# Performance work log

Hardware: AMD Instinct MI355X
Metric: run time of the kernel (lower is better)

## Reference

```python
import jax, jax.numpy as jnp
import numpy as np

B, S, D, H, V, DFF, L, MAXLEN = 256, 64, 1024, 16, 64, 4096, 8, 64
HD = D // H
SCALE = HD ** -0.5
EPS = 1e-5


def _ln(x, g, b):
    m = jnp.mean(x, axis=-1, keepdims=True)
    v = jnp.mean((x - m) ** 2, axis=-1, keepdims=True)
    return (x - m) * jax.lax.rsqrt(v + EPS) * g + b


def setup_inputs() -> dict:
    key = jax.random.key(0)
    ks = jax.random.split(key, 12)
    n = lambda k, shape: jax.random.normal(k, shape, jnp.float32) * 0.02
    return {
        "x": jax.random.randint(ks[0], (B, S), 0, V + 1),
        "step": 0,
        "token_embed": n(ks[1], (V + 1, D)),
        "step_embed": n(ks[2], (MAXLEN, D)),
        "qkv_w": n(ks[3], (L, 3 * D, D)),
        "qkv_b": jnp.zeros((L, 3 * D), jnp.float32),
        "out_w": n(ks[4], (L, D, D)),
        "out_b": jnp.zeros((L, D), jnp.float32),
        "rel_bias": n(ks[5], (L, 2 * MAXLEN - 1)),
        "w1": n(ks[6], (L, DFF, D)),
        "b1": jnp.zeros((L, DFF), jnp.float32),
        "w2": n(ks[7], (L, D, DFF)),
        "b2": jnp.zeros((L, D), jnp.float32),
        "ln1_g": jnp.ones((L, D), jnp.float32),
        "ln1_b": jnp.zeros((L, D), jnp.float32),
        "ln2_g": jnp.ones((L, D), jnp.float32),
        "ln2_b": jnp.zeros((L, D), jnp.float32),
        "lno_g": jnp.ones((D,), jnp.float32),
        "lno_b": jnp.zeros((D,), jnp.float32),
        "pol_w": n(ks[8], (V, D)),
        "pol_b": jnp.zeros((V,), jnp.float32),
        "val_w": n(ks[9], (1, D)),
        "val_b": jnp.zeros((1,), jnp.float32),
    }


def _forward(x, step, token_embed, step_embed, qkv_w, qkv_b, out_w, out_b,
             rel_bias, w1, b1, w2, b2, ln1_g, ln1_b, ln2_g, ln2_b,
             lno_g, lno_b, pol_w, pol_b, val_w, val_b):
    h = token_embed[x]  # [B,S,D]
    step_idx = min(int(step), MAXLEN - 1)
    h = h + step_embed[step_idx][None, None, :]

    pos = jnp.arange(S)
    rel_idx = jnp.clip(pos[:, None] - pos[None, :] + (MAXLEN - 1), 0, 2 * MAXLEN - 2)  # [S,S]

    def layer(h, p):
        qw, qb, ow, ob, rb, w1_, b1_, w2_, b2_, g1, be1, g2, be2 = p
        qkv = h @ qw.T + qb  # [B,S,3D]
        qkv = qkv.reshape(B, S, 3, H, HD).transpose(2, 0, 3, 1, 4)
        q, k, v = qkv[0], qkv[1], qkv[2]  # [B,H,S,HD]
        scores = jnp.einsum('bhqd,bhkd->bhqk', q, k) * SCALE + rb[rel_idx][None, None]
        probs = jax.nn.softmax(scores, axis=-1)
        attn = jnp.einsum('bhqk,bhkd->bhqd', probs, v)  # [B,H,S,HD]
        attn = attn.transpose(0, 2, 1, 3).reshape(B, S, D) @ ow.T + ob
        h = _ln(h + attn, g1, be1)
        ffn = jax.nn.gelu(h @ w1_.T + b1_, approximate=False) @ w2_.T + b2_
        h = _ln(h + ffn, g2, be2)
        return h, None

    h, _ = jax.lax.scan(layer, h, (qkv_w, qkv_b, out_w, out_b, rel_bias,
                                   w1, b1, w2, b2, ln1_g, ln1_b, ln2_g, ln2_b))
    h = _ln(h, lno_g, lno_b)
    pooled = h.mean(axis=1)  # [B,D]
    policy = pooled @ pol_w.T + pol_b  # [B,V]
    value = pooled @ val_w.T + val_b   # [B,1]
    return policy, value, h


def reference(x, step, token_embed, step_embed, qkv_w, qkv_b, out_w, out_b,
              rel_bias, w1, b1, w2, b2, ln1_g, ln1_b, ln2_g, ln2_b,
              lno_g, lno_b, pol_w, pol_b, val_w, val_b):
    return _forward(x, step, token_embed, step_embed, qkv_w, qkv_b, out_w, out_b,
                    rel_bias, w1, b1, w2, b2, ln1_g, ln1_b, ln2_g, ln2_b,
                    lno_g, lno_b, pol_w, pol_b, val_w, val_b)
```

## Files before the change

kernel.cpp:

```cpp
#include <hip/hip_runtime.h>
#include <math.h>

typedef _Float16 f16;
typedef _Float16 f16x8 __attribute__((ext_vector_type(8)));
typedef _Float16 f16x4 __attribute__((ext_vector_type(4)));
typedef float floatx4 __attribute__((ext_vector_type(4)));

#define BATCH 256
#define SEQ 64
#define DMODEL 1024
#define NHEAD 16
#define HDIM 64
#define VOCAB 64
#define DFF 4096
#define NLAYER 8
#define MS (BATCH*SEQ)

#define GPTR(p) ((const __attribute__((address_space(1))) void*)(p))
#define LPTR(p) ((__attribute__((address_space(3))) void*)(p))
#define GLDS(s, d) __builtin_amdgcn_global_load_lds(GPTR(s), LPTR(d), 16, 0, 0)
#define BARR() asm volatile("s_barrier" ::: "memory")

__device__ __forceinline__ floatx4 mfma16(f16x8 a, f16x8 b, floatx4 c) {
    return __builtin_amdgcn_mfma_f32_16x16x32_f16(a, b, c, 0, 0, 0);
}

__device__ __forceinline__ float gelu_f(float x) {
    float x3 = x * x * x;
    float y = -1.5957691216f * fmaf(0.044715f, x3, x);
    return x / (1.f + __expf(y));
}

__global__ __launch_bounds__(256) void embed_k(const int* __restrict__ x, const int* __restrict__ step,
                                               const float* __restrict__ tok, const float* __restrict__ se,
                                               f16* __restrict__ r) {
    int row = blockIdx.x;
    int t = threadIdx.x;
    int id = x[row];
    int si = min(max(step[0], 0), 63);
    float4 a = ((const float4*)(tok + (size_t)id * DMODEL))[t];
    float4 b = ((const float4*)(se + (size_t)si * DMODEL))[t];
    f16x4 hv; hv[0] = (f16)(a.x + b.x); hv[1] = (f16)(a.y + b.y);
    hv[2] = (f16)(a.z + b.z); hv[3] = (f16)(a.w + b.w);
    ((f16x4*)(r + (size_t)row * DMODEL))[t] = hv;
}

__global__ __launch_bounds__(256) void cvt4_k(const float* __restrict__ qw, const float* __restrict__ ow,
                                              const float* __restrict__ w1, const float* __restrict__ w2,
                                              f16* __restrict__ dq, f16* __restrict__ dO,
                                              f16* __restrict__ d1, f16* __restrict__ d2) {
    int gid = blockIdx.x * 256 + threadIdx.x;
    const float4* s; f16x4* d; int off;
    if (gid < 786432)        { s = (const float4*)qw; d = (f16x4*)dq; off = gid; }
    else if (gid < 1048576)  { s = (const float4*)ow; d = (f16x4*)dO; off = gid - 786432; }
    else if (gid < 2097152)  { s = (const float4*)w1; d = (f16x4*)d1; off = gid - 1048576; }
    else                     { s = (const float4*)w2; d = (f16x4*)d2; off = gid - 2097152; }
    float4 v = s[off];
    f16x4 o; o[0] = (f16)v.x; o[1] = (f16)v.y; o[2] = (f16)v.z; o[3] = (f16)v.w;
    d[off] = o;
}

template<int MODE>
__global__ __launch_bounds__(512, 2) void gemm8_k(const f16* __restrict__ A, const f16* __restrict__ Bw,
                                                  const float* __restrict__ bias, f16* __restrict__ Cb,
                                                  int M, int N, int K) {
    __shared__ f16 smem[65536];

    const int tid = threadIdx.x;
    const int lane = tid & 63;
    const int wave = tid >> 6;
    const int wm = wave >> 2, wn = wave & 3;
    const int lr = lane & 15, lg = lane >> 4;
    const int sa = lr & 7;

    const unsigned nx = gridDim.x;
    const unsigned nwg = nx * gridDim.y;
    unsigned flat = blockIdx.y * nx + blockIdx.x;
    flat = (flat & 7u) * (nwg >> 3) + (flat >> 3);
    const int m0 = (int)(flat / nx) * 256;
    const int n0 = (int)(flat % nx) * 256;

    floatx4 acc[8][4] = {};

    const int srow = tid >> 3;
    const int scb = (tid & 7) ^ (srow & 7);
    const f16* Ag = A + (size_t)(m0 + srow) * K + scb * 8;
    const f16* Bg = Bw + (size_t)(n0 + srow) * K + scb * 8;
    const int ldsw = wave * 512;

#define STAGE_A(bi, tt) do { const f16* _p = Ag + (size_t)(tt) * 64;                       \
    f16* _d = smem + (bi) * 32768 + ldsw;                                                  \
    GLDS(_p, _d); GLDS(_p + 64 * (size_t)K, _d + 4096);                                    \
    GLDS(_p + 128 * (size_t)K, _d + 8192); GLDS(_p + 192 * (size_t)K, _d + 12288); } while (0)
#define STAGE_BH(bi, tt, h) do { const f16* _p = Bg + (size_t)(tt) * 64 + (size_t)(h) * 128 * K; \
    f16* _d = smem + (bi) * 32768 + 16384 + (h) * 8192 + ldsw;                             \
    GLDS(_p, _d); GLDS(_p + 64 * (size_t)K, _d + 4096); } while (0)

    const int NT = K >> 6;

    STAGE_A(0, 0);
    STAGE_BH(0, 0, 0); STAGE_BH(0, 0, 1);
    STAGE_BH(1, 1, 0); STAGE_BH(1, 1, 1);
    asm volatile("s_waitcnt vmcnt(4)" ::: "memory");
    BARR();

    for (int t = 0; t < NT; ++t) {
        const int pofs = (t & 1) << 15;
        const f16* Ab = smem + pofs;
        const f16* Bb = smem + pofs + 16384;
        f16x8 bf[4][2];

        {
            f16x8 af[2][2];
#pragma unroll
            for (int kh = 0; kh < 2; ++kh)
#pragma unroll
                for (int i = 0; i < 2; ++i)
                    af[i][kh] = *(const f16x8*)(Ab + (wm * 128 + i * 16 + lr) * 64 + (((kh * 4 + lg) ^ sa) << 3));
#pragma unroll
            for (int kh = 0; kh < 2; ++kh)
#pragma unroll
                for (int ni = 0; ni < 4; ++ni)
                    bf[ni][kh] = *(const f16x8*)(Bb + (wn * 64 + ni * 16 + lr) * 64 + (((kh * 4 + lg) ^ sa) << 3));
            if (t + 1 < NT) STAGE_A((t & 1) ^ 1, t + 1);
            asm volatile("s_waitcnt lgkmcnt(8)" ::: "memory");
            BARR();
            asm volatile("s_waitcnt lgkmcnt(0)" ::: "memory");
            __builtin_amdgcn_sched_barrier(0);
            __builtin_amdgcn_s_setprio(1);
#pragma unroll
            for (int kh = 0; kh < 2; ++kh)
#pragma unroll
                for (int i = 0; i < 2; ++i)
#pragma unroll
                    for (int ni = 0; ni < 4; ++ni)
                        acc[i][ni] = mfma16(af[i][kh], bf[ni][kh], acc[i][ni]);
            __builtin_amdgcn_s_setprio(0);
            BARR();
        }
#pragma unroll
        for (int q = 1; q < 4; ++q) {
            f16x8 af[2][2];
#pragma unroll
            for (int kh = 0; kh < 2; ++kh)
#pragma unroll
                for (int i = 0; i < 2; ++i)
                    af[i][kh] = *(const f16x8*)(Ab + (wm * 128 + q * 32 + i * 16 + lr) * 64 + (((kh * 4 + lg) ^ sa) << 3));
            if (q == 1 && t + 2 < NT) STAGE_BH(t & 1, t + 2, 0);
            if (q == 2 && t + 2 < NT) STAGE_BH(t & 1, t + 2, 1);
            BARR();
            asm volatile("s_waitcnt lgkmcnt(0)" ::: "memory");
            __builtin_amdgcn_sched_barrier(0);
            __builtin_amdgcn_s_setprio(1);
#pragma unroll
            for (int kh = 0; kh < 2; ++kh)
#pragma unroll
                for (int i = 0; i < 2; ++i)
#pragma unroll
                    for (int ni = 0; ni < 4; ++ni)
                        acc[q * 2 + i][ni] = mfma16(af[i][kh], bf[ni][kh], acc[q * 2 + i][ni]);
            __builtin_amdgcn_s_setprio(0);
            if (q == 3) {
                if (t + 2 < NT)      { asm volatile("s_waitcnt vmcnt(4)" ::: "memory"); }
                else if (t + 1 < NT) { asm volatile("s_waitcnt vmcnt(0)" ::: "memory"); }
            }
            BARR();
        }
    }
#undef STAGE_A
#undef STAGE_BH

    f16* scr = smem + wave * 8192;
    float bsv[4];
#pragma unroll
    for (int ni = 0; ni < 4; ++ni) bsv[ni] = bias[n0 + wn * 64 + ni * 16 + lr];
#pragma unroll
    for (int mi = 0; mi < 8; ++mi)
#pragma unroll
        for (int ni = 0; ni < 4; ++ni)
#pragma unroll
            for (int j = 0; j < 4; ++j) {
                int rr = mi * 16 + lg * 4 + j;
                int cc = ni * 16 + lr;
                float v = acc[mi][ni][j] + bsv[ni];
                if (MODE == 1) v = gelu_f(v);
                scr[rr * 64 + (((cc >> 3) ^ (rr & 7)) * 8) + (cc & 7)] = (f16)v;
            }
#pragma unroll
    for (int half = 0; half < 2; ++half) {
        int r2 = half * 64 + lane;
        int gr = m0 + wm * 128 + r2;
        f16* dst = Cb + (size_t)gr * N + n0 + wn * 64;
#pragma unroll
        for (int i = 0; i < 8; ++i) {
            f16x8 v = *(const f16x8*)(scr + r2 * 64 + ((i ^ (r2 & 7)) * 8));
            *(f16x8*)(dst + i * 8) = v;
        }
    }
}

__global__ __launch_bounds__(256, 2) void gemm2_k(const f16* __restrict__ A, const f16* __restrict__ Bw,
                                                  const float* __restrict__ bias,
                                                  const f16* __restrict__ Rres, f16* __restrict__ ResOut,
                                                  float2* __restrict__ Part,
                                                  int M, int N, int K) {
    __shared__ f16 smem[40960];

    const int tid = threadIdx.x;
    const int lane = tid & 63;
    const int wave = tid >> 6;
    const int wm = wave >> 1, wn = wave & 1;
    const int lr = lane & 15, lg = lane >> 4;
    const int sa = lr & 7;

    const unsigned nx = gridDim.x;
    const unsigned nwg = nx * gridDim.y;
    unsigned flat = blockIdx.y * nx + blockIdx.x;
    flat = (flat & 7u) * (nwg >> 3) + (flat >> 3);
    const int m0 = (int)(flat / nx) * 128;
    const int n0 = (int)(flat % nx) * 128;

    floatx4 acc[4][4] = {};

    const int srow = tid >> 3;
    const int scbs = (tid & 7) ^ (srow & 7);
    const f16* Asrc = A + (size_t)(m0 + srow) * K + scbs * 8;
    const f16* Bsrc = Bw + (size_t)(n0 + srow) * K + scbs * 8;
    const int ldsw = wave * 512;

#define STAGEA(bi, tt) do { const f16* _a = Asrc + (size_t)(tt) * 64;                      \
    f16* _l = smem + (bi) * 8192 + ldsw;                                                   \
    GLDS(_a, _l); GLDS(_a + 32 * (size_t)K, _l + 2048);                                    \
    GLDS(_a + 64 * (size_t)K, _l + 4096); GLDS(_a + 96 * (size_t)K, _l + 6144); } while (0)
#define STAGEB(bi, tt) do { const f16* _b = Bsrc + (size_t)(tt) * 64;                      \
    f16* _l = smem + 16384 + (bi) * 8192 + ldsw;                                           \
    GLDS(_b, _l); GLDS(_b + 32 * (size_t)K, _l + 2048);                                    \
    GLDS(_b + 64 * (size_t)K, _l + 4096); GLDS(_b + 96 * (size_t)K, _l + 6144); } while (0)

    const int NT = K >> 6;

    STAGEA(0, 0);
    STAGEB(0, 0);
    STAGEB(1, 1);
    asm volatile("s_waitcnt vmcnt(4)" ::: "memory");
    __builtin_amdgcn_s_barrier();

    int ab = 0, bb = 0;
    for (int t = 0; t < NT; ++t) {
        if (t + 1 < NT) STAGEA(ab ^ 1, t + 1);
        if (t + 2 < NT) { int b2 = bb + 2; if (b2 >= 3) b2 -= 3; STAGEB(b2, t + 2); }

        const f16* Ab = smem + ab * 8192;
        const f16* Bb = smem + 16384 + bb * 8192;
        f16x8 af[8], bf[8];
#pragma unroll
        for (int kh = 0; kh < 2; ++kh)
#pragma unroll
            for (int mi = 0; mi < 4; ++mi)
                af[kh * 4 + mi] = *(const f16x8*)(Ab + (wm * 64 + mi * 16 + lr) * 64
                                                  + (((kh * 4 + lg) ^ sa) << 3));
#pragma unroll
        for (int kh = 0; kh < 2; ++kh)
#pragma unroll
            for (int ni = 0; ni < 4; ++ni)
                bf[kh * 4 + ni] = *(const f16x8*)(Bb + (wn * 64 + ni * 16 + lr) * 64
                                                  + (((kh * 4 + lg) ^ sa) << 3));

        __builtin_amdgcn_s_setprio(1);
#pragma unroll
        for (int kh = 0; kh < 2; ++kh)
#pragma unroll
            for (int mi = 0; mi < 4; ++mi)
#pragma unroll
                for (int ni = 0; ni < 4; ++ni)
                    acc[mi][ni] = mfma16(af[kh * 4 + mi], bf[kh * 4 + ni], acc[mi][ni]);
        __builtin_amdgcn_s_setprio(0);

        if (t + 2 < NT)      { asm volatile("s_waitcnt vmcnt(4)" ::: "memory"); }
        else if (t + 1 < NT) { asm volatile("s_waitcnt vmcnt(0)" ::: "memory"); }
        __builtin_amdgcn_s_barrier();

        ab ^= 1;
        bb = (bb == 2) ? 0 : bb + 1;
    }
#undef STAGEA
#undef STAGEB

    float bsv[4];
#pragma unroll
    for (int ni = 0; ni < 4; ++ni) bsv[ni] = bias[n0 + wn * 64 + ni * 16 + lr];
    f16* scr = smem + wave * 4096;
#pragma unroll
    for (int mi = 0; mi < 4; ++mi)
#pragma unroll
        for (int ni = 0; ni < 4; ++ni)
#pragma unroll
            for (int j = 0; j < 4; ++j) {
                int rr = mi * 16 + lg * 4 + j;
                int cc = ni * 16 + lr;
                scr[rr * 64 + (((cc >> 3) ^ (rr & 7)) * 8) + (cc & 7)]
                    = (f16)(acc[mi][ni][j] + bsv[ni]);
            }
    int gr = m0 + wm * 64 + lane;
    const f16* rrow = Rres + (size_t)gr * N + n0 + wn * 64;
    f16* orow = ResOut + (size_t)gr * N + n0 + wn * 64;
    float s = 0.f, ss = 0.f;
#pragma unroll
    for (int i = 0; i < 8; ++i) {
        f16x8 a = *(const f16x8*)(scr + lane * 64 + ((i ^ (lane & 7)) * 8));
        f16x8 rv = *(const f16x8*)(rrow + i * 8);
        f16x8 o;
#pragma unroll
        for (int k = 0; k < 8; ++k) {
            float v = (float)a[k] + (float)rv[k];
            s += v; ss += v * v;
            o[k] = (f16)v;
        }
        *(f16x8*)(orow + i * 8) = o;
    }
    float* red = (float*)(smem + 16384);
    if (wn == 1) { red[(wm * 64 + lane) * 2] = s; red[(wm * 64 + lane) * 2 + 1] = ss; }
    __syncthreads();
    if (wn == 0) {
        float s2 = red[(wm * 64 + lane) * 2], ss2 = red[(wm * 64 + lane) * 2 + 1];
        Part[(size_t)gr * (N >> 7) + (n0 >> 7)] = float2{s + s2, ss + ss2};
    }
}

__global__ __launch_bounds__(64) void attn_k(const f16* __restrict__ qkv, const float* __restrict__ rb,
                                             f16* __restrict__ ctx) {
    const int hh = blockIdx.x;
    const int bb = blockIdx.y;
    const int lane = threadIdx.x;
    __shared__ float rbs[128];
    __shared__ f16 Vt[64][72];
    __shared__ f16 Pl[64][72];

    for (int i = lane; i < 127; i += 64) rbs[i] = rb[i];

    const f16* vrow = qkv + (size_t)(bb * 64 + lane) * 3072 + 2048 + hh * 64;
#pragma unroll
    for (int i = 0; i < 8; ++i) {
        f16x8 v = *(const f16x8*)(vrow + i * 8);
#pragma unroll
        for (int j = 0; j < 8; ++j) Vt[i * 8 + j][lane] = v[j];
    }
    __syncthreads();

    const int lr = lane & 15, lg = lane >> 4;
    floatx4 sacc[4][4] = {};
    const f16* qbase = qkv + (size_t)(bb * 64) * 3072 + hh * 64;
#pragma unroll
    for (int kk = 0; kk < 64; kk += 32) {
        f16x8 qa[4], kb[4];
#pragma unroll
        for (int mf = 0; mf < 4; ++mf)
            qa[mf] = *(const f16x8*)(qbase + (size_t)(mf * 16 + lr) * 3072 + kk + lg * 8);
#pragma unroll
        for (int nf = 0; nf < 4; ++nf)
            kb[nf] = *(const f16x8*)(qbase + 1024 + (size_t)(nf * 16 + lr) * 3072 + kk + lg * 8);
#pragma unroll
        for (int mf = 0; mf < 4; ++mf)
#pragma unroll
            for (int nf = 0; nf < 4; ++nf)
                sacc[mf][nf] = mfma16(qa[mf], kb[nf], sacc[mf][nf]);
    }

#pragma unroll
    for (int mf = 0; mf < 4; ++mf) {
#pragma unroll
        for (int j = 0; j < 4; ++j) {
            int qrow = mf * 16 + lg * 4 + j;
            float v0 = sacc[mf][0][j] * 0.125f + rbs[qrow - (0  + lr) + 63];
            float v1 = sacc[mf][1][j] * 0.125f + rbs[qrow - (16 + lr) + 63];
            float v2 = sacc[mf][2][j] * 0.125f + rbs[qrow - (32 + lr) + 63];
            float v3 = sacc[mf][3][j] * 0.125f + rbs[qrow - (48 + lr) + 63];
            float mx = fmaxf(fmaxf(v0, v1), fmaxf(v2, v3));
            for (int m = 1; m < 16; m <<= 1) mx = fmaxf(mx, __shfl_xor(mx, m));
            v0 = __expf(v0 - mx); v1 = __expf(v1 - mx); v2 = __expf(v2 - mx); v3 = __expf(v3 - mx);
            float sum = v0 + v1 + v2 + v3;
            for (int m = 1; m < 16; m <<= 1) sum += __shfl_xor(sum, m);
            float inv = 1.f / sum;
            Pl[qrow][0  + lr] = (f16)(v0 * inv);
            Pl[qrow][16 + lr] = (f16)(v1 * inv);
            Pl[qrow][32 + lr] = (f16)(v2 * inv);
            Pl[qrow][48 + lr] = (f16)(v3 * inv);
        }
    }
    __syncthreads();

    floatx4 oacc[4][4] = {};
#pragma unroll
    for (int kk = 0; kk < 64; kk += 32) {
        f16x8 pa[4], vb[4];
#pragma unroll
        for (int mf = 0; mf < 4; ++mf) pa[mf] = *(const f16x8*)&Pl[mf * 16 + lr][kk + lg * 8];
#pragma unroll
        for (int nf = 0; nf < 4; ++nf) vb[nf] = *(const f16x8*)&Vt[nf * 16 + lr][kk + lg * 8];
#pragma unroll
        for (int mf = 0; mf < 4; ++mf)
#pragma unroll
            for (int nf = 0; nf < 4; ++nf)
                oacc[mf][nf] = mfma16(pa[mf], vb[nf], oacc[mf][nf]);
    }
    __syncthreads();
#pragma unroll
    for (int mf = 0; mf < 4; ++mf)
#pragma unroll
        for (int nf = 0; nf < 4; ++nf)
#pragma unroll
            for (int j = 0; j < 4; ++j)
                Pl[mf * 16 + lg * 4 + j][nf * 16 + lr] = (f16)oacc[mf][nf][j];
    __syncthreads();
    f16* crow = ctx + (size_t)(bb * 64 + lane) * DMODEL + hh * 64;
#pragma unroll
    for (int i = 0; i < 8; ++i) {
        f16x8 v = *(const f16x8*)&Pl[lane][i * 8];
        *(f16x8*)(crow + i * 8) = v;
    }
}

__global__ __launch_bounds__(128) void ln_k(const f16* __restrict__ res, const float2* __restrict__ part,
                                            const float* __restrict__ g, const float* __restrict__ b,
                                            f16* __restrict__ out) {
    int row = blockIdx.x;
    int t = threadIdx.x;
    f16x8 rv = ((const f16x8*)(res + (size_t)row * DMODEL))[t];
    float s = 0.f, ss = 0.f;
#pragma unroll
    for (int c = 0; c < 8; ++c) {
        float2 p = part[(size_t)row * 8 + c];
        s += p.x; ss += p.y;
    }
    float mean = s * (1.f / 1024.f);
    float var = ss * (1.f / 1024.f) - mean * mean;
    float rstd = rsqrtf(var + 1e-5f);
    float4 g0 = ((const float4*)g)[t * 2], g1 = ((const float4*)g)[t * 2 + 1];
    float4 b0 = ((const float4*)b)[t * 2], b1 = ((const float4*)b)[t * 2 + 1];
    f16x8 o;
    o[0] = (f16)(((float)rv[0] - mean) * rstd * g0.x + b0.x);
    o[1] = (f16)(((float)rv[1] - mean) * rstd * g0.y + b0.y);
    o[2] = (f16)(((float)rv[2] - mean) * rstd * g0.z + b0.z);
    o[3] = (f16)(((float)rv[3] - mean) * rstd * g0.w + b0.w);
    o[4] = (f16)(((float)rv[4] - mean) * rstd * g1.x + b1.x);
    o[5] = (f16)(((float)rv[5] - mean) * rstd * g1.y + b1.y);
    o[6] = (f16)(((float)rv[6] - mean) * rstd * g1.z + b1.z);
    o[7] = (f16)(((float)rv[7] - mean) * rstd * g1.w + b1.w);
    ((f16x8*)(out + (size_t)row * DMODEL))[t] = o;
}

__global__ __launch_bounds__(256) void lnf_k(const f16* __restrict__ res, const float* __restrict__ g,
                                             const float* __restrict__ b, float* __restrict__ h) {
    int row = blockIdx.x;
    int t = threadIdx.x;
    f16x4 rv = ((const f16x4*)(res + (size_t)row * DMODEL))[t];
    float v0 = (float)rv[0], v1 = (float)rv[1], v2 = (float)rv[2], v3 = (float)rv[3];
    float s = v0 + v1 + v2 + v3;
    float ss = v0 * v0 + v1 * v1 + v2 * v2 + v3 * v3;
    for (int m = 1; m < 64; m <<= 1) { s += __shfl_xor(s, m); ss += __shfl_xor(ss, m); }
    __shared__ float red[8];
    if ((t & 63) == 0) { red[(t >> 6) * 2] = s; red[(t >> 6) * 2 + 1] = ss; }
    __syncthreads();
    s = red[0] + red[2] + red[4] + red[6];
    ss = red[1] + red[3] + red[5] + red[7];
    float mean = s * (1.f / 1024.f);
    float var = ss * (1.f / 1024.f) - mean * mean;
    float rstd = rsqrtf(var + 1e-5f);
    float4 gg = ((const float4*)g)[t];
    float4 bb = ((const float4*)b)[t];
    float4 o;
    o.x = (v0 - mean) * rstd * gg.x + bb.x;
    o.y = (v1 - mean) * rstd * gg.y + bb.y;
    o.z = (v2 - mean) * rstd * gg.z + bb.z;
    o.w = (v3 - mean) * rstd * gg.w + bb.w;
    ((float4*)(h + (size_t)row * DMODEL))[t] = o;
}

__global__ __launch_bounds__(256) void pool_k(const float* __restrict__ h, float* __restrict__ pooled) {
    int b = blockIdx.x;
    int t = threadIdx.x;
    float sx = 0, sy = 0, sz = 0, sw = 0;
    for (int s = 0; s < SEQ; ++s) {
        float4 v = ((const float4*)(h + (size_t)(b * SEQ + s) * DMODEL))[t];
        sx += v.x; sy += v.y; sz += v.z; sw += v.w;
    }
    float4 o; o.x = sx * (1.f / 64.f); o.y = sy * (1.f / 64.f); o.z = sz * (1.f / 64.f); o.w = sw * (1.f / 64.f);
    ((float4*)(pooled + (size_t)b * DMODEL))[t] = o;
}

__global__ __launch_bounds__(64) void head_k(const float* __restrict__ pooled, const float* __restrict__ pw,
                                             const float* __restrict__ pb, const float* __restrict__ vw,
                                             const float* __restrict__ vb, float* __restrict__ out) {
    int b = blockIdx.x;
    int lane = threadIdx.x;
    const float* pr = pooled + (size_t)b * DMODEL;
    const float* wr = pw + (size_t)lane * DMODEL;
    float accp = 0.f;
    for (int d = 0; d < DMODEL; d += 4) {
        float4 x = *(const float4*)(pr + d);
        float4 w = *(const float4*)(wr + d);
        accp += x.x * w.x + x.y * w.y + x.z * w.z + x.w * w.w;
    }
    float accv = 0.f;
    for (int d = lane * 4; d < DMODEL; d += 256) {
        float4 x = *(const float4*)(pr + d);
        float4 w = *(const float4*)(vw + d);
        accv += x.x * w.x + x.y * w.y + x.z * w.z + x.w * w.w;
    }
    for (int m = 1; m < 64; m <<= 1) accv += __shfl_xor(accv, m);
    out[b * VOCAB + lane] = accp + pb[lane];
    if (lane == 0) out[BATCH * VOCAB + b] = accv + vb[0];
}

extern "C" void kernel_launch(void* const* d_in, const int* in_sizes, int n_in,
                              void* d_out, int out_size, void* d_ws, size_t ws_size,
                              hipStream_t stream) {
    const int*   x      = (const int*)d_in[0];
    const int*   step   = (const int*)d_in[1];
    const float* tok    = (const float*)d_in[2];
    const float* se     = (const float*)d_in[3];
    const float* qkv_w  = (const float*)d_in[4];
    const float* qkv_b  = (const float*)d_in[5];
    const float* out_w  = (const float*)d_in[6];
    const float* out_b  = (const float*)d_in[7];
    const float* relb   = (const float*)d_in[8];
    const float* w1     = (const float*)d_in[9];
    const float* b1     = (const float*)d_in[10];
    const float* w2     = (const float*)d_in[11];
    const float* b2     = (const float*)d_in[12];
    const float* ln1g   = (const float*)d_in[13];
    const float* ln1b   = (const float*)d_in[14];
    const float* ln2g   = (const float*)d_in[15];
    const float* ln2b   = (const float*)d_in[16];
    const float* lnog   = (const float*)d_in[17];
    const float* lnob   = (const float*)d_in[18];
    const float* pw     = (const float*)d_in[19];
    const float* pb     = (const float*)d_in[20];
    const float* vw     = (const float*)d_in[21];
    const float* vb     = (const float*)d_in[22];

    float* out = (float*)d_out;
    float* h = out + BATCH * VOCAB + BATCH;

    char* ws = (char*)d_ws;
    f16* rB     = (f16*)(ws);
    f16* resA   = (f16*)(ws + 33554432);
    f16* qkv16  = (f16*)(ws + 67108864);
    f16* ctx16  = (f16*)(ws + 167772160);
    f16* ffn16  = (f16*)(ws + 67108864);
    f16* wqb    = (f16*)(ws + 201326592);
    f16* wob    = (f16*)(ws + 207618048);
    f16* w1b    = (f16*)(ws + 209715200);
    f16* w2b    = (f16*)(ws + 218103808);
    float2* part = (float2*)(ws + 226492416);
    float* pooled = (float*)(ws + 226492416);

    embed_k<<<MS, 256, 0, stream>>>(x, step, tok, se, rB);

    for (int l = 0; l < NLAYER; ++l) {
        cvt4_k<<<12288, 256, 0, stream>>>(qkv_w + (size_t)l * 3145728, out_w + (size_t)l * 1048576,
                                          w1 + (size_t)l * 4194304, w2 + (size_t)l * 4194304,
                                          wqb, wob, w1b, w2b);

        gemm8_k<0><<<dim3(12, 64), 512, 0, stream>>>(rB, wqb, qkv_b + l * 3072, qkv16, MS, 3072, 1024);
        attn_k<<<dim3(NHEAD, BATCH), 64, 0, stream>>>(qkv16, relb + l * 127, ctx16);
        gemm2_k<<<dim3(8, 128), 256, 0, stream>>>(ctx16, wob, out_b + l * 1024,
                                                  rB, resA, part, MS, 1024, 1024);
        ln_k<<<MS, 128, 0, stream>>>(resA, part, ln1g + l * 1024, ln1b + l * 1024, rB);
        gemm8_k<1><<<dim3(16, 64), 512, 0, stream>>>(rB, w1b, b1 + l * 4096, ffn16, MS, 4096, 1024);
        gemm2_k<<<dim3(8, 128), 256, 0, stream>>>(ffn16, w2b, b2 + l * 1024,
                                                  rB, resA, part, MS, 1024, 4096);
        ln_k<<<MS, 128, 0, stream>>>(resA, part, ln2g + l * 1024, ln2b + l * 1024, rB);
    }

    lnf_k<<<MS, 256, 0, stream>>>(rB, lnog, lnob, h);
    pool_k<<<BATCH, 256, 0, stream>>>(h, pooled);
    head_k<<<BATCH, 64, 0, stream>>>(pooled, pw, pb, vw, vb, out);
}
```

Baseline: 4.675 ms.

## Swap GEMM tile sizes: 256x256 for residual GEMMs, 128x128 for FFN1

The out-projection and FFN2 GEMMs (N=1024) now use the large 256x256 tile kernel, which gains a fused residual-add and partial-LayerNorm-statistics epilogue. The FFN1 GEMM with GELU moves to the 128x128 tile kernel, which gains a plain-store GELU epilogue. The aim is more operand reuse on the residual GEMMs and better wave balance across the GPU. The trade-off is that the N=1024 GEMMs launch only 256 workgroups, which may underfill the device.

```diff
diff --git a/kernel.cpp b/kernel.cpp
--- a/kernel.cpp
+++ b/kernel.cpp
@@ -63,6 +63,8 @@
 template<int MODE>
 __global__ __launch_bounds__(512, 2) void gemm8_k(const f16* __restrict__ A, const f16* __restrict__ Bw,
                                                   const float* __restrict__ bias, f16* __restrict__ Cb,
+                                                  const f16* __restrict__ Rres, f16* __restrict__ ResOut,
+                                                  float2* __restrict__ Part,
                                                   int M, int N, int K) {
     __shared__ f16 smem[65536];
 
@@ -183,27 +185,62 @@
                 int rr = mi * 16 + lg * 4 + j;
                 int cc = ni * 16 + lr;
                 float v = acc[mi][ni][j] + bsv[ni];
-                if (MODE == 1) v = gelu_f(v);
                 scr[rr * 64 + (((cc >> 3) ^ (rr & 7)) * 8) + (cc & 7)] = (f16)v;
             }
-#pragma unroll
-    for (int half = 0; half < 2; ++half) {
-        int r2 = half * 64 + lane;
-        int gr = m0 + wm * 128 + r2;
-        f16* dst = Cb + (size_t)gr * N + n0 + wn * 64;
-#pragma unroll
-        for (int i = 0; i < 8; ++i) {
-            f16x8 v = *(const f16x8*)(scr + r2 * 64 + ((i ^ (r2 & 7)) * 8));
-            *(f16x8*)(dst + i * 8) = v;
+    if (MODE == 0) {
+#pragma unroll
+        for (int half = 0; half < 2; ++half) {
+            int r2 = half * 64 + lane;
+            int gr = m0 + wm * 128 + r2;
+            f16* dst = Cb + (size_t)gr * N + n0 + wn * 64;
+#pragma unroll
+            for (int i = 0; i < 8; ++i) {
+                f16x8 v = *(const f16x8*)(scr + r2 * 64 + ((i ^ (r2 & 7)) * 8));
+                *(f16x8*)(dst + i * 8) = v;
+            }
         }
-    }
-}
-
-__global__ __launch_bounds__(256, 2) void gemm2_k(const f16* __restrict__ A, const f16* __restrict__ Bw,
-                                                  const float* __restrict__ bias,
-                                                  const f16* __restrict__ Rres, f16* __restrict__ ResOut,
-                                                  float2* __restrict__ Part,
-                                                  int M, int N, int K) {
+    } else {
+        float sh[2], ssh[2];
+#pragma unroll
+        for (int half = 0; half < 2; ++half) {
+            int r2 = half * 64 + lane;
+            int gr = m0 + wm * 128 + r2;
+            const f16* rrow = Rres + (size_t)gr * N + n0 + wn * 64;
+            f16* orow = ResOut + (size_t)gr * N + n0 + wn * 64;
+            float s = 0.f, ss = 0.f;
+#pragma unroll
+            for (int i = 0; i < 8; ++i) {
+                f16x8 a = *(const f16x8*)(scr + r2 * 64 + ((i ^ (r2 & 7)) * 8));
+                f16x8 rv = *(const f16x8*)(rrow + i * 8);
+                f16x8 o;
+#pragma unroll
+                for (int k = 0; k < 8; ++k) {
+                    float v = (float)a[k] + (float)rv[k];
+                    s += v; ss += v * v;
+                    o[k] = (f16)v;
+                }
+                *(f16x8*)(orow + i * 8) = o;
+            }
+            sh[half] = s; ssh[half] = ss;
+        }
+        __syncthreads();
+        float2* red = (float2*)smem;
+#pragma unroll
+        for (int half = 0; half < 2; ++half)
+            red[(wm * 128 + half * 64 + lane) * 4 + wn] = float2{sh[half], ssh[half]};
+        __syncthreads();
+        {
+            int row = tid >> 1, ch = tid & 1;
+            float2 p0 = red[row * 4 + 2 * ch], p1 = red[row * 4 + 2 * ch + 1];
+            Part[(size_t)(m0 + row) * (N >> 7) + (n0 >> 7) + ch] = float2{p0.x + p1.x, p0.y + p1.y};
+        }
+    }
+}
+
+template<int MODE>
+__global__ __launch_bounds__(256, 2) void gemm_k(const f16* __restrict__ A, const f16* __restrict__ Bw,
+                                                 const float* __restrict__ bias,
+                                                 f16* __restrict__ Cb, int M, int N, int K) {
     __shared__ f16 smem[40960];
 
     const int tid = threadIdx.x;
@@ -286,10 +323,10 @@
 #undef STAGEA
 #undef STAGEB
 
+    f16* scr = smem + wave * 4096;
     float bsv[4];
 #pragma unroll
     for (int ni = 0; ni < 4; ++ni) bsv[ni] = bias[n0 + wn * 64 + ni * 16 + lr];
-    f16* scr = smem + wave * 4096;
 #pragma unroll
     for (int mi = 0; mi < 4; ++mi)
 #pragma unroll
@@ -298,32 +335,16 @@
             for (int j = 0; j < 4; ++j) {
                 int rr = mi * 16 + lg * 4 + j;
                 int cc = ni * 16 + lr;
-                scr[rr * 64 + (((cc >> 3) ^ (rr & 7)) * 8) + (cc & 7)]
-                    = (f16)(acc[mi][ni][j] + bsv[ni]);
+                float v = acc[mi][ni][j] + bsv[ni];
+                if (MODE == 1) v = gelu_f(v);
+                scr[rr * 64 + (((cc >> 3) ^ (rr & 7)) * 8) + (cc & 7)] = (f16)v;
             }
     int gr = m0 + wm * 64 + lane;
-    const f16* rrow = Rres + (size_t)gr * N + n0 + wn * 64;
-    f16* orow = ResOut + (size_t)gr * N + n0 + wn * 64;
-    float s = 0.f, ss = 0.f;
+    f16* dst = Cb + (size_t)gr * N + n0 + wn * 64;
 #pragma unroll
     for (int i = 0; i < 8; ++i) {
-        f16x8 a = *(const f16x8*)(scr + lane * 64 + ((i ^ (lane & 7)) * 8));
-        f16x8 rv = *(const f16x8*)(rrow + i * 8);
-        f16x8 o;
-#pragma unroll
-        for (int k = 0; k < 8; ++k) {
-            float v = (float)a[k] + (float)rv[k];
-            s += v; ss += v * v;
-            o[k] = (f16)v;
-        }
-        *(f16x8*)(orow + i * 8) = o;
-    }
-    float* red = (float*)(smem + 16384);
-    if (wn == 1) { red[(wm * 64 + lane) * 2] = s; red[(wm * 64 + lane) * 2 + 1] = ss; }
-    __syncthreads();
-    if (wn == 0) {
-        float s2 = red[(wm * 64 + lane) * 2], ss2 = red[(wm * 64 + lane) * 2 + 1];
-        Part[(size_t)gr * (N >> 7) + (n0 >> 7)] = float2{s + s2, ss + ss2};
+        f16x8 v = *(const f16x8*)(scr + lane * 64 + ((i ^ (lane & 7)) * 8));
+        *(f16x8*)(dst + i * 8) = v;
     }
 }
 
@@ -562,14 +583,15 @@
                                           w1 + (size_t)l * 4194304, w2 + (size_t)l * 4194304,
                                           wqb, wob, w1b, w2b);
 
-        gemm8_k<0><<<dim3(12, 64), 512, 0, stream>>>(rB, wqb, qkv_b + l * 3072, qkv16, MS, 3072, 1024);
+        gemm8_k<0><<<dim3(12, 64), 512, 0, stream>>>(rB, wqb, qkv_b + l * 3072, qkv16,
+                                                     nullptr, nullptr, nullptr, MS, 3072, 1024);
         attn_k<<<dim3(NHEAD, BATCH), 64, 0, stream>>>(qkv16, relb + l * 127, ctx16);
-        gemm2_k<<<dim3(8, 128), 256, 0, stream>>>(ctx16, wob, out_b + l * 1024,
-                                                  rB, resA, part, MS, 1024, 1024);
+        gemm8_k<2><<<dim3(4, 64), 512, 0, stream>>>(ctx16, wob, out_b + l * 1024, nullptr,
+                                                    rB, resA, part, MS, 1024, 1024);
         ln_k<<<MS, 128, 0, stream>>>(resA, part, ln1g + l * 1024, ln1b + l * 1024, rB);
-        gemm8_k<1><<<dim3(16, 64), 512, 0, stream>>>(rB, w1b, b1 + l * 4096, ffn16, MS, 4096, 1024);
-        gemm2_k<<<dim3(8, 128), 256, 0, stream>>>(ffn16, w2b, b2 + l * 1024,
-                                                  rB, resA, part, MS, 1024, 4096);
+        gemm_k<1><<<dim3(32, 128), 256, 0, stream>>>(rB, w1b, b1 + l * 4096, ffn16, MS, 4096, 1024);
+        gemm8_k<2><<<dim3(4, 64), 512, 0, stream>>>(ffn16, w2b, b2 + l * 1024, nullptr,
+                                                    rB, resA, part, MS, 1024, 4096);
         ln_k<<<MS, 128, 0, stream>>>(resA, part, ln2g + l * 1024, ln2b + l * 1024, rB);
     }
 
```

Result: slower. 4.991 ms (+6.7%).
